# Kernel tuning notes

Measured on AMD Instinct MI355X. Metric: run time of the kernel, lower is better.

## Reference

```python
import jax, jax.numpy as jnp
import numpy as np
from jax import lax

N_NEURONS = 2500
K = 50
T = 60
F = 5
H = 128
GROUP_SIZES = [800, 700, 600, 400]  # support_resistance, trend, pattern, volume
GID = jnp.asarray(np.repeat(np.arange(4), GROUP_SIZES))  # [N] specialty id per neuron
_BOUNDS = np.cumsum([0] + GROUP_SIZES)


def _lstm_layer(x, w_ih, w_hh, b_ih, b_hh):
    # x: [B,T,in]; PyTorch gate order i,f,g,o in the 4H weight rows
    B = x.shape[0]
    Hd = w_hh.shape[1]
    def step(carry, xt):
        h, c = carry
        g = xt @ w_ih.T + h @ w_hh.T + b_ih + b_hh
        i, f, gg, o = jnp.split(g, 4, axis=-1)
        c = jax.nn.sigmoid(f) * c + jax.nn.sigmoid(i) * jnp.tanh(gg)
        h = jax.nn.sigmoid(o) * jnp.tanh(c)
        return (h, c), h
    init = (jnp.zeros((B, Hd), x.dtype), jnp.zeros((B, Hd), x.dtype))
    (h, _), ys = lax.scan(step, init, jnp.swapaxes(x, 0, 1))
    return jnp.swapaxes(ys, 0, 1), h


def _forward(x, w_ih0, w_hh0, b_ih0, b_hh0, w_ih1, w_hh1, b_ih1, b_hh1,
             pw1, pb1, pw2, pb2, conn_w, sens, thr,
             iw1, ib1, iw2, ib2, iw3, ib3,
             hw_trend, hb_trend, hw_pat, hb_pat, hw_key, hb_key,
             hw_vol, hb_vol, hw_conf, hb_conf, conn_idx):
    seq, _ = _lstm_layer(x, w_ih0, w_hh0, b_ih0, b_hh0)
    _, h2 = _lstm_layer(seq, w_ih1, w_hh1, b_ih1, b_hh1)  # hidden[-1]: [B,H]
    # feature_projection: Linear->ReLU->Linear->Tanh
    base = jnp.tanh(jax.nn.relu(h2 @ pw1.T + pb1) @ pw2.T + pb2)  # [B,32]
    # broadcast base features to a per-neuron activation vector [B,N]
    reps = -(-N_NEURONS // base.shape[1])
    all_act = jnp.tile(base, (1, reps))[:, :N_NEURONS]
    # batched sparse gather + per-neuron weighted sum
    gathered = all_act[:, conn_idx]                       # [B,N,K]
    z = jnp.einsum('bnk,nk->bn', gathered, conn_w) * sens  # [B,N]
    # specialty-conditioned activation
    a = jnp.where(GID == 0, jax.nn.sigmoid(z - thr),
        jnp.where(GID == 1, jnp.tanh(z),
        jnp.where(GID == 2, jax.nn.relu(z - thr), jax.nn.sigmoid(z))))
    # integrator (dropout is eval-mode no-op)
    integ = jnp.tanh(jax.nn.relu(jax.nn.relu(a @ iw1.T + ib1) @ iw2.T + ib2) @ iw3.T + ib3)
    trend = integ @ hw_trend.T + hb_trend      # [B,3]
    pat = integ @ hw_pat.T + hb_pat            # [B,6]
    key_l = integ @ hw_key.T + hb_key          # [B,4]
    vol = integ @ hw_vol.T + hb_vol            # [B,1]
    conf = integ @ hw_conf.T + hb_conf         # [B,1]
    overall = jax.nn.sigmoid(conf)             # [B,1]
    means = jnp.stack([a[:, _BOUNDS[i]:_BOUNDS[i + 1]].mean(axis=1) for i in range(4)], axis=1)
    return jnp.concatenate([trend, pat, key_l, vol, conf, overall, means], axis=1)  # [B,20]


def setup_inputs() -> dict:
    key = jax.random.key(0)
    ks = iter(jax.random.split(key, 64))
    def rn(shape, s=0.05):
        return jax.random.normal(next(ks), shape, jnp.float32) * s
    B = 1024
    return {
        'x': jax.random.normal(next(ks), (B, T, F), jnp.float32),
        'conn_idx': jax.random.randint(next(ks), (N_NEURONS, K), 0, N_NEURONS, jnp.int32),
        'w_ih0': rn((4 * H, F)), 'w_hh0': rn((4 * H, H)),
        'b_ih0': rn((4 * H,), 0.01), 'b_hh0': rn((4 * H,), 0.01),
        'w_ih1': rn((4 * H, H)), 'w_hh1': rn((4 * H, H)),
        'b_ih1': rn((4 * H,), 0.01), 'b_hh1': rn((4 * H,), 0.01),
        'pw1': rn((64, H)), 'pb1': rn((64,), 0.01),
        'pw2': rn((32, 64)), 'pb2': rn((32,), 0.01),
        'conn_w': rn((N_NEURONS, K), 0.1),
        'sens': rn((N_NEURONS,), 0.1) + 1.0,
        'thr': rn((N_NEURONS,), 0.1) + 0.6,
        'iw1': rn((256, N_NEURONS), 0.01), 'ib1': rn((256,), 0.01),
        'iw2': rn((64, 256)), 'ib2': rn((64,), 0.01),
        'iw3': rn((32, 64)), 'ib3': rn((32,), 0.01),
        'hw_trend': rn((3, 32)), 'hb_trend': rn((3,), 0.01),
        'hw_pat': rn((6, 32)), 'hb_pat': rn((6,), 0.01),
        'hw_key': rn((4, 32)), 'hb_key': rn((4,), 0.01),
        'hw_vol': rn((1, 32)), 'hb_vol': rn((1,), 0.01),
        'hw_conf': rn((1, 32)), 'hb_conf': rn((1,), 0.01),
    }


def reference(x, conn_idx, w_ih0, w_hh0, b_ih0, b_hh0, w_ih1, w_hh1, b_ih1, b_hh1,
              pw1, pb1, pw2, pb2, conn_w, sens, thr,
              iw1, ib1, iw2, ib2, iw3, ib3,
              hw_trend, hb_trend, hw_pat, hb_pat, hw_key, hb_key,
              hw_vol, hb_vol, hw_conf, hb_conf):
    return _forward(x, w_ih0, w_hh0, b_ih0, b_hh0, w_ih1, w_hh1, b_ih1, b_hh1,
                    pw1, pb1, pw2, pb2, conn_w, sens, thr,
                    iw1, ib1, iw2, ib2, iw3, ib3,
                    hw_trend, hb_trend, hw_pat, hb_pat, hw_key, hb_key,
                    hw_vol, hb_vol, hw_conf, hb_conf, conn_idx)
```

## Files before the change

### kernel.cpp

```cpp
#include <hip/hip_runtime.h>
#include <hip/hip_bf16.h>
#include <math.h>

#define DEV __device__ __forceinline__

typedef short short8 __attribute__((ext_vector_type(8)));
typedef float f32x4  __attribute__((ext_vector_type(4)));

DEV float sigf(float x)   { return 1.0f / (1.0f + __expf(-x)); }
DEV float tanhft(float x) { return 1.0f - 2.0f / (__expf(2.0f * x) + 1.0f); }

DEV unsigned short f2bf(float f) {
    unsigned int u = __float_as_uint(f);
    unsigned int r = (u + 0x7FFFu + ((u >> 16) & 1u)) >> 16;
    return (unsigned short)r;
}
DEV float bf2f(unsigned short u) {
    return __uint_as_float(((unsigned int)u) << 16);
}

DEV void bar_lds() {
    asm volatile("s_waitcnt lgkmcnt(0)" ::: "memory");
    __builtin_amdgcn_s_barrier();
}

__global__ __launch_bounds__(256) void prep_kernel(
    const float* __restrict__ w_hh0, const float* __restrict__ w_ih1,
    const float* __restrict__ w_hh1,
    const float* __restrict__ b_ih0, const float* __restrict__ b_hh0,
    const float* __restrict__ b_ih1, const float* __restrict__ b_hh1,
    unsigned short* __restrict__ whh0h, unsigned short* __restrict__ wih1h,
    unsigned short* __restrict__ whh1h,
    float* __restrict__ bias0, float* __restrict__ bias1)
{
    int i = blockIdx.x * 256 + threadIdx.x;
    if (i < 65536) {
        whh0h[i] = f2bf(w_hh0[i]);
        wih1h[i] = f2bf(w_ih1[i]);
        whh1h[i] = f2bf(w_hh1[i]);
    } else if (i < 66048) {
        int c = i - 65536;
        bias0[c] = b_ih0[c] + b_hh0[c];
        bias1[c] = b_ih1[c] + b_hh1[c];
    }
}

__global__ __launch_bounds__(256) void prep_iw1_kernel(
    const float* __restrict__ iw1, unsigned short* __restrict__ iw1b)
{
    int i = blockIdx.x * 256 + threadIdx.x;
    if (i < 256 * 2528) {
        int row = i / 2528, k = i - row * 2528;
        iw1b[i] = (k < 2500) ? f2bf(iw1[row * 2500 + k]) : (unsigned short)0;
    }
}

__global__ __launch_bounds__(512, 2) void lstm_kernel(
    const float* __restrict__ x,
    const unsigned short* __restrict__ whh0,
    const unsigned short* __restrict__ wih1,
    const unsigned short* __restrict__ whh1,
    const float* __restrict__ wih0,
    const float* __restrict__ bias0, const float* __restrict__ bias1,
    float* __restrict__ h2out)
{
    __shared__ __align__(16) float          xs[4][304];
    __shared__ __align__(16) unsigned short h0s[2][16][136];
    __shared__ __align__(16) unsigned short h1s[2][16][136];
    __shared__ __align__(16) float          wsc[8][4][16][4];
    __shared__ float wih0s[2560];

    const int tid = threadIdx.x;
    const int b0  = blockIdx.x * 4;
    const int l15 = tid & 15;
    const int q   = (tid >> 4) & 3;
    const int w   = tid >> 6;
    const int j   = w * 16 + l15;
    const int q8  = q * 8;

    for (int i = tid; i < 1200; i += 512) {
        int m = i / 300, kk = i - m * 300;
        xs[m][kk] = x[(b0 + m) * 300 + kk];
    }
    for (int i = tid; i < 2560; i += 512) wih0s[i] = wih0[i];
    for (int i = tid; i < 2176; i += 512) {
        ((unsigned int*)h0s)[i] = 0u;
        ((unsigned int*)h1s)[i] = 0u;
    }

    float ub0[4], ub1[4];
#pragma unroll
    for (int g = 0; g < 4; ++g) {
        ub0[g] = bias0[g * 128 + j];
        ub1[g] = bias1[g * 128 + j];
    }

    short8 bh0[4][4], b1i[4][4];
#pragma unroll
    for (int g = 0; g < 4; ++g)
#pragma unroll
        for (int kc = 0; kc < 4; ++kc) {
            int off = (g * 128 + j) * 128 + kc * 32 + q8;
            bh0[g][kc] = *(const short8*)(whh0 + off);
            b1i[g][kc] = *(const short8*)(wih1 + off);
        }

    float c0 = 0.f, c1 = 0.f, hl = 0.f;
    __syncthreads();

    const unsigned short* wsb = whh1 + j * 128 + q8;

    for (int t = 0; t < 60; ++t) {
        const int p = t & 1;

        short8 wsv[4][4];
#pragma unroll
        for (int g = 0; g < 4; ++g) {
            wsv[g][0] = *(const short8*)(wsb + g * 16384);
            wsv[g][1] = *(const short8*)(wsb + g * 16384 + 32);
        }

        f32x4 acc[4];
#pragma unroll
        for (int g = 0; g < 4; ++g) acc[g] = (f32x4){0.f, 0.f, 0.f, 0.f};
        short8 af[4];
#pragma unroll
        for (int kc = 0; kc < 4; ++kc)
            af[kc] = *(const short8*)&h0s[p][l15][kc * 32 + q8];
#pragma unroll
        for (int kc = 0; kc < 4; ++kc)
#pragma unroll
            for (int g = 0; g < 4; ++g)
                acc[g] = __builtin_amdgcn_mfma_f32_16x16x32_bf16(af[kc], bh0[g][kc], acc[g], 0, 0, 0);

#pragma unroll
        for (int g = 0; g < 4; ++g) {
            wsv[g][2] = *(const short8*)(wsb + g * 16384 + 64);
            wsv[g][3] = *(const short8*)(wsb + g * 16384 + 96);
        }

        if (q == 0) {
#pragma unroll
            for (int g = 0; g < 4; ++g)
                *(f32x4*)&wsc[w][g][l15][0] = acc[g];
        }
        {
            const float* xr = &xs[q][t * 5];
            float x0 = xr[0], x1 = xr[1], x2 = xr[2], x3 = xr[3], x4 = xr[4];
            float gv[4];
#pragma unroll
            for (int g = 0; g < 4; ++g) {
                const float* wr = &wih0s[(g * 128 + j) * 5];
                float s = wsc[w][g][l15][q] + ub0[g];
                s = fmaf(x0, wr[0], s);
                s = fmaf(x1, wr[1], s);
                s = fmaf(x2, wr[2], s);
                s = fmaf(x3, wr[3], s);
                gv[g] = fmaf(x4, wr[4], s);
            }
            c0 = sigf(gv[1]) * c0 + sigf(gv[0]) * tanhft(gv[2]);
            float h = sigf(gv[3]) * tanhft(c0);
            h0s[1 - p][q][j] = f2bf(h);
        }

        bar_lds();

#pragma unroll
        for (int g = 0; g < 4; ++g) acc[g] = (f32x4){0.f, 0.f, 0.f, 0.f};
#pragma unroll
        for (int kc = 0; kc < 4; ++kc)
            af[kc] = *(const short8*)&h0s[1 - p][l15][kc * 32 + q8];
#pragma unroll
        for (int kc = 0; kc < 4; ++kc)
#pragma unroll
            for (int g = 0; g < 4; ++g)
                acc[g] = __builtin_amdgcn_mfma_f32_16x16x32_bf16(af[kc], b1i[g][kc], acc[g], 0, 0, 0);
#pragma unroll
        for (int kc = 0; kc < 4; ++kc)
            af[kc] = *(const short8*)&h1s[p][l15][kc * 32 + q8];
#pragma unroll
        for (int kc = 0; kc < 4; ++kc)
#pragma unroll
            for (int g = 0; g < 4; ++g)
                acc[g] = __builtin_amdgcn_mfma_f32_16x16x32_bf16(af[kc], wsv[g][kc], acc[g], 0, 0, 0);

        if (q == 0) {
#pragma unroll
            for (int g = 0; g < 4; ++g)
                *(f32x4*)&wsc[w][g][l15][0] = acc[g];
        }
        {
            float gv[4];
#pragma unroll
            for (int g = 0; g < 4; ++g)
                gv[g] = wsc[w][g][l15][q] + ub1[g];
            c1 = sigf(gv[1]) * c1 + sigf(gv[0]) * tanhft(gv[2]);
            float h = sigf(gv[3]) * tanhft(c1);
            h1s[1 - p][q][j] = f2bf(h);
            hl = h;
        }
    }

    h2out[(b0 + q) * 128 + j] = hl;
}

__global__ __launch_bounds__(256) void phase2_kernel(
    const float* __restrict__ h2, const float* __restrict__ pw1,
    const float* __restrict__ pb1, const float* __restrict__ pw2,
    const float* __restrict__ pb2, float* __restrict__ base)
{
    __shared__ float pw1s[64 * 129];
    __shared__ float pw2s[32 * 65];
    __shared__ float hs[4][128];
    __shared__ float p1s[4][64];

    const int tid = threadIdx.x;
    const int b0  = blockIdx.x * 4;

    for (int i = tid; i < 8192; i += 256) {
        int u = i >> 7, k = i & 127;
        pw1s[u * 129 + k] = pw1[i];
    }
    for (int i = tid; i < 2048; i += 256) {
        int u = i >> 6, k = i & 63;
        pw2s[u * 65 + k] = pw2[i];
    }
    for (int i = tid; i < 512; i += 256)
        hs[i >> 7][i & 127] = h2[b0 * 128 + i];
    __syncthreads();

    {
        const int r = tid >> 6, u = tid & 63;
        float acc = pb1[u];
        const float* wr = &pw1s[u * 129];
        const float* hr = &hs[r][0];
#pragma unroll 4
        for (int k = 0; k < 128; ++k) acc = fmaf(hr[k], wr[k], acc);
        p1s[r][u] = fmaxf(acc, 0.f);
    }
    __syncthreads();

    if (tid < 128) {
        const int r = tid >> 5, u2 = tid & 31;
        float a2 = pb2[u2];
        const float* wr = &pw2s[u2 * 65];
        const float* pr = &p1s[r][0];
#pragma unroll 4
        for (int k = 0; k < 64; ++k) a2 = fmaf(pr[k], wr[k], a2);
        base[(b0 + r) * 32 + u2] = tanhft(a2);
    }
}

__global__ __launch_bounds__(128) void weff_kernel(
    const int* __restrict__ conn_idx, const float* __restrict__ conn_w,
    float* __restrict__ weffT)
{
    __shared__ float s[128 * 33];
    int tid = threadIdx.x;
    int n = blockIdx.x * 128 + tid;
    float* sr = &s[tid * 33];
#pragma unroll
    for (int j = 0; j < 32; ++j) sr[j] = 0.f;
    if (n < 2500) {
        for (int k = 0; k < 50; ++k) {
            int idx = conn_idx[n * 50 + k];
            sr[idx & 31] += conn_w[n * 50 + k];
        }
        for (int j = 0; j < 32; ++j) weffT[j * 2500 + n] = sr[j];
    }
}

__global__ __launch_bounds__(256) void za_kernel(
    const float* __restrict__ base, const float* __restrict__ weffT,
    const float* __restrict__ sens, const float* __restrict__ thr,
    unsigned short* __restrict__ amat)
{
    __shared__ float bs[16][32];
    int tid = threadIdx.x;
    int bb = blockIdx.x / 10, nb = blockIdx.x % 10;
    int n = nb * 256 + tid;
    bool nv = n < 2500;
    bool pv = n < 2528;
    int nn = nv ? n : 0;
    for (int i = tid; i < 512; i += 256) bs[i >> 5][i & 31] = base[bb * 512 + i];
    __syncthreads();
    float w[32];
#pragma unroll
    for (int j = 0; j < 32; ++j) w[j] = weffT[j * 2500 + nn];
    float sn = sens[nn], tn = thr[nn];
    int g = (n < 800) ? 0 : (n < 1500) ? 1 : (n < 2100) ? 2 : 3;
#pragma unroll 2
    for (int r = 0; r < 16; ++r) {
        float z = 0.f;
#pragma unroll
        for (int j = 0; j < 32; ++j) z = fmaf(bs[r][j], w[j], z);
        z *= sn;
        float av;
        if (g == 0)      av = sigf(z - tn);
        else if (g == 1) av = tanhft(z);
        else if (g == 2) av = fmaxf(z - tn, 0.f);
        else             av = sigf(z);
        if (nv)      amat[(bb * 16 + r) * 2528 + n] = f2bf(av);
        else if (pv) amat[(bb * 16 + r) * 2528 + n] = 0;
    }
}

__global__ __launch_bounds__(128) void gemm_iw1_kernel(
    const unsigned short* __restrict__ ab, const unsigned short* __restrict__ wb,
    const float* __restrict__ ib1, float* __restrict__ t1)
{
    const int tid = threadIdx.x;
    const int wv  = tid >> 6;
    const int l15 = tid & 15, q = (tid >> 4) & 3, q8 = q * 8;
    const int row0 = blockIdx.y * 32 + wv * 16;
    const int col0 = blockIdx.x * 32;

    const unsigned short* A = ab + (row0 + l15) * 2528 + q8;
    const unsigned short* B = wb + (col0 + l15) * 2528 + q8;

    short8 a = *(const short8*)A;
    short8 b[2];
#pragma unroll
    for (int nt = 0; nt < 2; ++nt) b[nt] = *(const short8*)(B + nt * 16 * 2528);

    f32x4 acc[2];
#pragma unroll
    for (int nt = 0; nt < 2; ++nt) acc[nt] = (f32x4){0.f, 0.f, 0.f, 0.f};

    for (int c = 0; c < 79; ++c) {
        int cn = (c < 78) ? c + 1 : 78;
        short8 an = *(const short8*)(A + cn * 32);
        short8 bn[2];
#pragma unroll
        for (int nt = 0; nt < 2; ++nt)
            bn[nt] = *(const short8*)(B + nt * 16 * 2528 + cn * 32);
#pragma unroll
        for (int nt = 0; nt < 2; ++nt)
            acc[nt] = __builtin_amdgcn_mfma_f32_16x16x32_bf16(a, b[nt], acc[nt], 0, 0, 0);
        a = an;
#pragma unroll
        for (int nt = 0; nt < 2; ++nt) b[nt] = bn[nt];
    }

#pragma unroll
    for (int nt = 0; nt < 2; ++nt) {
        int n = col0 + nt * 16 + l15;
        float bias = ib1[n];
#pragma unroll
        for (int i = 0; i < 4; ++i) {
            int row = row0 + q * 4 + i;
            t1[row * 256 + n] = fmaxf(acc[nt][i] + bias, 0.f);
        }
    }
}

__global__ __launch_bounds__(256) void final_kernel(
    const float* __restrict__ t1, const float* __restrict__ iw2,
    const float* __restrict__ ib2, const float* __restrict__ iw3,
    const float* __restrict__ ib3,
    const float* __restrict__ hw_trend, const float* __restrict__ hb_trend,
    const float* __restrict__ hw_pat,   const float* __restrict__ hb_pat,
    const float* __restrict__ hw_key,   const float* __restrict__ hb_key,
    const float* __restrict__ hw_vol,   const float* __restrict__ hb_vol,
    const float* __restrict__ hw_conf,  const float* __restrict__ hb_conf,
    float* __restrict__ out)
{
    __shared__ float iw2s[64 * 257];
    __shared__ float iw3s[32 * 65];
    __shared__ float t1s[4][256];
    __shared__ float t2s[4][64];
    __shared__ float igs[4][32];

    const int tid = threadIdx.x;
    const int b0  = blockIdx.x * 4;

    for (int i = tid; i < 16384; i += 256) {
        int u = i >> 8, k = i & 255;
        iw2s[u * 257 + k] = iw2[i];
    }
    for (int i = tid; i < 2048; i += 256) {
        int u = i >> 6, k = i & 63;
        iw3s[u * 65 + k] = iw3[i];
    }
    for (int i = tid; i < 1024; i += 256)
        t1s[i >> 8][i & 255] = t1[b0 * 256 + i];
    __syncthreads();

    {
        const int r = tid >> 6, u = tid & 63;
        float acc = ib2[u];
        const float* wr = &iw2s[u * 257];
        const float* tr = &t1s[r][0];
#pragma unroll 4
        for (int k = 0; k < 256; ++k) acc = fmaf(tr[k], wr[k], acc);
        t2s[r][u] = fmaxf(acc, 0.f);
    }
    __syncthreads();

    if (tid < 128) {
        const int r = tid >> 5, u2 = tid & 31;
        float a2 = ib3[u2];
        const float* wr = &iw3s[u2 * 65];
        const float* tr = &t2s[r][0];
#pragma unroll 4
        for (int k = 0; k < 64; ++k) a2 = fmaf(tr[k], wr[k], a2);
        igs[r][u2] = tanhft(a2);
    }
    __syncthreads();

    if (tid < 60) {
        const int r = tid / 15, t15 = tid % 15;
        const int b = b0 + r;
        const float* w; const float* bb; int j, off;
        if (t15 < 3)        { w = hw_trend; bb = hb_trend; j = t15;     off = 0; }
        else if (t15 < 9)   { w = hw_pat;   bb = hb_pat;   j = t15 - 3; off = 3; }
        else if (t15 < 13)  { w = hw_key;   bb = hb_key;   j = t15 - 9; off = 9; }
        else if (t15 == 13) { w = hw_vol;   bb = hb_vol;   j = 0;       off = 13; }
        else                { w = hw_conf;  bb = hb_conf;  j = 0;       off = 14; }
        float a3 = bb[j];
#pragma unroll
        for (int k = 0; k < 32; ++k) a3 = fmaf(igs[r][k], w[j * 32 + k], a3);
        out[b * 20 + off + j] = a3;
        if (t15 == 14) out[b * 20 + 15] = sigf(a3);
    }
}

__global__ __launch_bounds__(256) void means_kernel(
    const unsigned short* __restrict__ amat, float* __restrict__ out)
{
    __shared__ float red[16];
    int b = blockIdx.x, tid = threadIdx.x;
    float parts[4] = {0.f, 0.f, 0.f, 0.f};
    for (int n0 = tid * 8; n0 < 2500; n0 += 2048) {
        short8 v = *(const short8*)(amat + b * 2528 + n0);
#pragma unroll
        for (int e = 0; e < 8; ++e) {
            int n = n0 + e;
            float f = bf2f((unsigned short)v[e]);
            if (n < 800)       parts[0] += f;
            else if (n < 1500) parts[1] += f;
            else if (n < 2100) parts[2] += f;
            else               parts[3] += f;
        }
    }
    int lane = tid & 63, wv = tid >> 6;
#pragma unroll
    for (int g = 0; g < 4; ++g) {
        float v = parts[g];
        for (int s = 32; s > 0; s >>= 1) v += __shfl_down(v, s, 64);
        if (lane == 0) red[wv * 4 + g] = v;
    }
    __syncthreads();
    if (tid < 4) {
        float s = red[tid] + red[4 + tid] + red[8 + tid] + red[12 + tid];
        float invg = (tid == 0) ? (1.f / 800.f) : (tid == 1) ? (1.f / 700.f)
                   : (tid == 2) ? (1.f / 600.f) : (1.f / 400.f);
        out[b * 20 + 16 + tid] = s * invg;
    }
}

extern "C" void kernel_launch(void* const* d_in, const int* in_sizes, int n_in,
                              void* d_out, int out_size, void* d_ws, size_t ws_size,
                              hipStream_t stream)
{
    const float* x        = (const float*)d_in[0];
    const int*   conn_idx = (const int*)  d_in[1];
    const float* w_ih0    = (const float*)d_in[2];
    const float* w_hh0    = (const float*)d_in[3];
    const float* b_ih0    = (const float*)d_in[4];
    const float* b_hh0    = (const float*)d_in[5];
    const float* w_ih1    = (const float*)d_in[6];
    const float* w_hh1    = (const float*)d_in[7];
    const float* b_ih1    = (const float*)d_in[8];
    const float* b_hh1    = (const float*)d_in[9];
    const float* pw1      = (const float*)d_in[10];
    const float* pb1      = (const float*)d_in[11];
    const float* pw2      = (const float*)d_in[12];
    const float* pb2      = (const float*)d_in[13];
    const float* conn_w   = (const float*)d_in[14];
    const float* sens     = (const float*)d_in[15];
    const float* thr      = (const float*)d_in[16];
    const float* iw1      = (const float*)d_in[17];
    const float* ib1      = (const float*)d_in[18];
    const float* iw2      = (const float*)d_in[19];
    const float* ib2      = (const float*)d_in[20];
    const float* iw3      = (const float*)d_in[21];
    const float* ib3      = (const float*)d_in[22];
    const float* hw_trend = (const float*)d_in[23];
    const float* hb_trend = (const float*)d_in[24];
    const float* hw_pat   = (const float*)d_in[25];
    const float* hb_pat   = (const float*)d_in[26];
    const float* hw_key   = (const float*)d_in[27];
    const float* hb_key   = (const float*)d_in[28];
    const float* hw_vol   = (const float*)d_in[29];
    const float* hb_vol   = (const float*)d_in[30];
    const float* hw_conf  = (const float*)d_in[31];
    const float* hb_conf  = (const float*)d_in[32];
    float* out = (float*)d_out;
    float* ws  = (float*)d_ws;

    unsigned short* whh0h = (unsigned short*)(ws);
    unsigned short* wih1h = (unsigned short*)(ws + 32768);
    unsigned short* whh1h = (unsigned short*)(ws + 65536);
    float* bias0  = ws + 98304;
    float* bias1  = ws + 98816;
    float* h2     = ws + 99328;
    float* base_  = ws + 230400;
    float* weffT  = ws + 263168;
    float* t1     = ws + 343168;
    unsigned short* iw1b   = (unsigned short*)(ws + 605312);
    unsigned short* amatbf = (unsigned short*)(ws + 928896);

    prep_kernel<<<258, 256, 0, stream>>>(w_hh0, w_ih1, w_hh1,
                                         b_ih0, b_hh0, b_ih1, b_hh1,
                                         whh0h, wih1h, whh1h, bias0, bias1);
    prep_iw1_kernel<<<2528, 256, 0, stream>>>(iw1, iw1b);
    lstm_kernel<<<256, 512, 0, stream>>>(x, whh0h, wih1h, whh1h, w_ih0,
                                         bias0, bias1, h2);
    phase2_kernel<<<256, 256, 0, stream>>>(h2, pw1, pb1, pw2, pb2, base_);
    weff_kernel<<<20, 128, 0, stream>>>(conn_idx, conn_w, weffT);
    za_kernel<<<640, 256, 0, stream>>>(base_, weffT, sens, thr, amatbf);
    gemm_iw1_kernel<<<dim3(8, 32), 128, 0, stream>>>(amatbf, iw1b, ib1, t1);
    final_kernel<<<256, 256, 0, stream>>>(t1, iw2, ib2, iw3, ib3,
                                          hw_trend, hb_trend, hw_pat, hb_pat,
                                          hw_key, hb_key, hw_vol, hb_vol,
                                          hw_conf, hb_conf, out);
    means_kernel<<<1024, 256, 0, stream>>>(amatbf, out);
}
```

Before: 294.9 us.

## Split LSTM layers across wave groups and pipeline layer 1 one step behind

Waves 0-3 now compute only layer 0 and waves 4-7 compute only layer 1, which runs one timestep behind. Each step needs a single barrier instead of two serialized layer phases. Each wave covers 32 hidden units with two MFMA column tiles. Layer-1 waves reload whh1 and wih1 from global memory every step to keep register use bounded, which adds global/L2 traffic and risks stalls on the critical path.

```diff
diff --git a/kernel.cpp b/kernel.cpp
--- a/kernel.cpp
+++ b/kernel.cpp
@@ -67,16 +67,24 @@
     __shared__ __align__(16) float          xs[4][304];
     __shared__ __align__(16) unsigned short h0s[2][16][136];
     __shared__ __align__(16) unsigned short h1s[2][16][136];
-    __shared__ __align__(16) float          wsc[8][4][16][4];
+    __shared__ __align__(16) float          wsc[8][4][2][16][4];
     __shared__ float wih0s[2560];
 
-    const int tid = threadIdx.x;
-    const int b0  = blockIdx.x * 4;
-    const int l15 = tid & 15;
-    const int q   = (tid >> 4) & 3;
-    const int w   = tid >> 6;
-    const int j   = w * 16 + l15;
-    const int q8  = q * 8;
+    const int tid  = threadIdx.x;
+    const int b0   = blockIdx.x * 4;
+    const int l15  = tid & 15;
+    const int q    = (tid >> 4) & 3;
+    const int w    = tid >> 6;
+    const int q8   = q * 8;
+    const int lane = tid & 63;
+    const int w4   = w & 3;
+    const bool isL0 = (w < 4);
+
+    const int uloc  = lane & 31;
+    const int unit  = w4 * 32 + uloc;
+    const int ct    = uloc >> 4;
+    const int col   = uloc & 15;
+    const int rbase = (lane >> 5) * 2;
 
     for (int i = tid; i < 1200; i += 512) {
         int m = i / 300, kk = i - m * 300;
@@ -88,120 +96,157 @@
         ((unsigned int*)h1s)[i] = 0u;
     }
 
-    float ub0[4], ub1[4];
-#pragma unroll
-    for (int g = 0; g < 4; ++g) {
-        ub0[g] = bias0[g * 128 + j];
-        ub1[g] = bias1[g * 128 + j];
-    }
-
-    short8 bh0[4][4], b1i[4][4];
+    float ub[4];
 #pragma unroll
     for (int g = 0; g < 4; ++g)
-#pragma unroll
-        for (int kc = 0; kc < 4; ++kc) {
-            int off = (g * 128 + j) * 128 + kc * 32 + q8;
-            bh0[g][kc] = *(const short8*)(whh0 + off);
-            b1i[g][kc] = *(const short8*)(wih1 + off);
+        ub[g] = isL0 ? bias0[g * 128 + unit] : bias1[g * 128 + unit];
+
+    short8 wreg[4][2][4];
+    {
+        const unsigned short* src = isL0 ? whh0 : wih1;
+#pragma unroll
+        for (int g = 0; g < 4; ++g)
+#pragma unroll
+            for (int c2 = 0; c2 < 2; ++c2)
+#pragma unroll
+                for (int kc = 0; kc < 4; ++kc)
+                    wreg[g][c2][kc] = *(const short8*)(src
+                        + (g * 128 + w4 * 32 + c2 * 16 + l15) * 128 + kc * 32 + q8);
+    }
+    const unsigned short* sWhh1 = whh1 + (w4 * 32 + l15) * 128 + q8;
+    const unsigned short* sWih1 = wih1 + (w4 * 32 + l15) * 128 + q8;
+
+    float cA = 0.f, cB = 0.f;
+    float hlA = 0.f, hlB = 0.f;
+    __syncthreads();
+
+    for (int i = 0; i <= 60; ++i) {
+        const int pi = i & 1;
+
+        if (isL0) {
+            if (i < 60) {
+                short8 af[4];
+#pragma unroll
+                for (int kc = 0; kc < 4; ++kc)
+                    af[kc] = *(const short8*)&h0s[pi][l15][kc * 32 + q8];
+                f32x4 acc[4][2];
+#pragma unroll
+                for (int g = 0; g < 4; ++g) {
+                    acc[g][0] = (f32x4){0.f, 0.f, 0.f, 0.f};
+                    acc[g][1] = (f32x4){0.f, 0.f, 0.f, 0.f};
+                }
+#pragma unroll
+                for (int kc = 0; kc < 4; ++kc)
+#pragma unroll
+                    for (int g = 0; g < 4; ++g) {
+                        acc[g][0] = __builtin_amdgcn_mfma_f32_16x16x32_bf16(af[kc], wreg[g][0][kc], acc[g][0], 0, 0, 0);
+                        acc[g][1] = __builtin_amdgcn_mfma_f32_16x16x32_bf16(af[kc], wreg[g][1][kc], acc[g][1], 0, 0, 0);
+                    }
+                if (q == 0) {
+#pragma unroll
+                    for (int g = 0; g < 4; ++g) {
+                        *(f32x4*)&wsc[w][g][0][l15][0] = acc[g][0];
+                        *(f32x4*)&wsc[w][g][1][l15][0] = acc[g][1];
+                    }
+                }
+                const float* xr0 = &xs[rbase][i * 5];
+                const float* xr1 = &xs[rbase + 1][i * 5];
+                float gv0[4], gv1[4];
+#pragma unroll
+                for (int g = 0; g < 4; ++g) {
+                    const float* wr = &wih0s[(g * 128 + unit) * 5];
+                    float w0 = wr[0], w1 = wr[1], w2 = wr[2], w3 = wr[3], w4v = wr[4];
+                    float s0 = wsc[w][g][ct][col][rbase]     + ub[g];
+                    float s1 = wsc[w][g][ct][col][rbase + 1] + ub[g];
+                    s0 = fmaf(xr0[0], w0, s0); s1 = fmaf(xr1[0], w0, s1);
+                    s0 = fmaf(xr0[1], w1, s0); s1 = fmaf(xr1[1], w1, s1);
+                    s0 = fmaf(xr0[2], w2, s0); s1 = fmaf(xr1[2], w2, s1);
+                    s0 = fmaf(xr0[3], w3, s0); s1 = fmaf(xr1[3], w3, s1);
+                    gv0[g] = fmaf(xr0[4], w4v, s0);
+                    gv1[g] = fmaf(xr1[4], w4v, s1);
+                }
+                cA = sigf(gv0[1]) * cA + sigf(gv0[0]) * tanhft(gv0[2]);
+                float hA = sigf(gv0[3]) * tanhft(cA);
+                h0s[1 - pi][rbase][unit] = f2bf(hA);
+                cB = sigf(gv1[1]) * cB + sigf(gv1[0]) * tanhft(gv1[2]);
+                float hB = sigf(gv1[3]) * tanhft(cB);
+                h0s[1 - pi][rbase + 1][unit] = f2bf(hB);
+            }
+        } else {
+            if (i >= 1) {
+                short8 af[4];
+#pragma unroll
+                for (int kc = 0; kc < 4; ++kc)
+                    af[kc] = *(const short8*)&h0s[pi][l15][kc * 32 + q8];
+                f32x4 acc[4][2];
+#pragma unroll
+                for (int g = 0; g < 4; ++g) {
+                    acc[g][0] = (f32x4){0.f, 0.f, 0.f, 0.f};
+                    acc[g][1] = (f32x4){0.f, 0.f, 0.f, 0.f};
+                }
+#pragma unroll
+                for (int kc = 0; kc < 4; ++kc)
+#pragma unroll
+                    for (int g = 0; g < 4; ++g) {
+                        acc[g][0] = __builtin_amdgcn_mfma_f32_16x16x32_bf16(af[kc], wreg[g][0][kc], acc[g][0], 0, 0, 0);
+                        acc[g][1] = __builtin_amdgcn_mfma_f32_16x16x32_bf16(af[kc], wreg[g][1][kc], acc[g][1], 0, 0, 0);
+                    }
+#pragma unroll
+                for (int g = 0; g < 4; ++g)
+#pragma unroll
+                    for (int c2 = 0; c2 < 2; ++c2)
+#pragma unroll
+                        for (int kc = 0; kc < 4; ++kc)
+                            wreg[g][c2][kc] = *(const short8*)(sWhh1
+                                + (g * 128 + c2 * 16) * 128 + kc * 32);
+                short8 af2[4];
+#pragma unroll
+                for (int kc = 0; kc < 4; ++kc)
+                    af2[kc] = *(const short8*)&h1s[1 - pi][l15][kc * 32 + q8];
+#pragma unroll
+                for (int kc = 0; kc < 4; ++kc)
+#pragma unroll
+                    for (int g = 0; g < 4; ++g) {
+                        acc[g][0] = __builtin_amdgcn_mfma_f32_16x16x32_bf16(af2[kc], wreg[g][0][kc], acc[g][0], 0, 0, 0);
+                        acc[g][1] = __builtin_amdgcn_mfma_f32_16x16x32_bf16(af2[kc], wreg[g][1][kc], acc[g][1], 0, 0, 0);
+                    }
+#pragma unroll
+                for (int g = 0; g < 4; ++g)
+#pragma unroll
+                    for (int c2 = 0; c2 < 2; ++c2)
+#pragma unroll
+                        for (int kc = 0; kc < 4; ++kc)
+                            wreg[g][c2][kc] = *(const short8*)(sWih1
+                                + (g * 128 + c2 * 16) * 128 + kc * 32);
+                if (q == 0) {
+#pragma unroll
+                    for (int g = 0; g < 4; ++g) {
+                        *(f32x4*)&wsc[w][g][0][l15][0] = acc[g][0];
+                        *(f32x4*)&wsc[w][g][1][l15][0] = acc[g][1];
+                    }
+                }
+                float gv0[4], gv1[4];
+#pragma unroll
+                for (int g = 0; g < 4; ++g) {
+                    gv0[g] = wsc[w][g][ct][col][rbase]     + ub[g];
+                    gv1[g] = wsc[w][g][ct][col][rbase + 1] + ub[g];
+                }
+                cA = sigf(gv0[1]) * cA + sigf(gv0[0]) * tanhft(gv0[2]);
+                hlA = sigf(gv0[3]) * tanhft(cA);
+                h1s[pi][rbase][unit] = f2bf(hlA);
+                cB = sigf(gv1[1]) * cB + sigf(gv1[0]) * tanhft(gv1[2]);
+                hlB = sigf(gv1[3]) * tanhft(cB);
+                h1s[pi][rbase + 1][unit] = f2bf(hlB);
+            }
         }
 
-    float c0 = 0.f, c1 = 0.f, hl = 0.f;
-    __syncthreads();
-
-    const unsigned short* wsb = whh1 + j * 128 + q8;
-
-    for (int t = 0; t < 60; ++t) {
-        const int p = t & 1;
-
-        short8 wsv[4][4];
-#pragma unroll
-        for (int g = 0; g < 4; ++g) {
-            wsv[g][0] = *(const short8*)(wsb + g * 16384);
-            wsv[g][1] = *(const short8*)(wsb + g * 16384 + 32);
-        }
-
-        f32x4 acc[4];
-#pragma unroll
-        for (int g = 0; g < 4; ++g) acc[g] = (f32x4){0.f, 0.f, 0.f, 0.f};
-        short8 af[4];
-#pragma unroll
-        for (int kc = 0; kc < 4; ++kc)
-            af[kc] = *(const short8*)&h0s[p][l15][kc * 32 + q8];
-#pragma unroll
-        for (int kc = 0; kc < 4; ++kc)
-#pragma unroll
-            for (int g = 0; g < 4; ++g)
-                acc[g] = __builtin_amdgcn_mfma_f32_16x16x32_bf16(af[kc], bh0[g][kc], acc[g], 0, 0, 0);
-
-#pragma unroll
-        for (int g = 0; g < 4; ++g) {
-            wsv[g][2] = *(const short8*)(wsb + g * 16384 + 64);
-            wsv[g][3] = *(const short8*)(wsb + g * 16384 + 96);
-        }
-
-        if (q == 0) {
-#pragma unroll
-            for (int g = 0; g < 4; ++g)
-                *(f32x4*)&wsc[w][g][l15][0] = acc[g];
-        }
-        {
-            const float* xr = &xs[q][t * 5];
-            float x0 = xr[0], x1 = xr[1], x2 = xr[2], x3 = xr[3], x4 = xr[4];
-            float gv[4];
-#pragma unroll
-            for (int g = 0; g < 4; ++g) {
-                const float* wr = &wih0s[(g * 128 + j) * 5];
-                float s = wsc[w][g][l15][q] + ub0[g];
-                s = fmaf(x0, wr[0], s);
-                s = fmaf(x1, wr[1], s);
-                s = fmaf(x2, wr[2], s);
-                s = fmaf(x3, wr[3], s);
-                gv[g] = fmaf(x4, wr[4], s);
-            }
-            c0 = sigf(gv[1]) * c0 + sigf(gv[0]) * tanhft(gv[2]);
-            float h = sigf(gv[3]) * tanhft(c0);
-            h0s[1 - p][q][j] = f2bf(h);
-        }
-
         bar_lds();
-
-#pragma unroll
-        for (int g = 0; g < 4; ++g) acc[g] = (f32x4){0.f, 0.f, 0.f, 0.f};
-#pragma unroll
-        for (int kc = 0; kc < 4; ++kc)
-            af[kc] = *(const short8*)&h0s[1 - p][l15][kc * 32 + q8];
-#pragma unroll
-        for (int kc = 0; kc < 4; ++kc)
-#pragma unroll
-            for (int g = 0; g < 4; ++g)
-                acc[g] = __builtin_amdgcn_mfma_f32_16x16x32_bf16(af[kc], b1i[g][kc], acc[g], 0, 0, 0);
-#pragma unroll
-        for (int kc = 0; kc < 4; ++kc)
-            af[kc] = *(const short8*)&h1s[p][l15][kc * 32 + q8];
-#pragma unroll
-        for (int kc = 0; kc < 4; ++kc)
-#pragma unroll
-            for (int g = 0; g < 4; ++g)
-                acc[g] = __builtin_amdgcn_mfma_f32_16x16x32_bf16(af[kc], wsv[g][kc], acc[g], 0, 0, 0);
-
-        if (q == 0) {
-#pragma unroll
-            for (int g = 0; g < 4; ++g)
-                *(f32x4*)&wsc[w][g][l15][0] = acc[g];
-        }
-        {
-            float gv[4];
-#pragma unroll
-            for (int g = 0; g < 4; ++g)
-                gv[g] = wsc[w][g][l15][q] + ub1[g];
-            c1 = sigf(gv[1]) * c1 + sigf(gv[0]) * tanhft(gv[2]);
-            float h = sigf(gv[3]) * tanhft(c1);
-            h1s[1 - p][q][j] = f2bf(h);
-            hl = h;
-        }
-    }
-
-    h2out[(b0 + q) * 128 + j] = hl;
+    }
+
+    if (!isL0) {
+        h2out[(b0 + rbase) * 128 + unit]     = hlA;
+        h2out[(b0 + rbase + 1) * 128 + unit] = hlB;
+    }
 }
 
 __global__ __launch_bounds__(256) void phase2_kernel(
```

After: 750.3 us. +154.5%, slower.
